# Kernel tuning notes

Hardware: AMD Instinct MI355X
Metric: run time of the kernel (lower is better)

The kernel has to match this reference:

```python
import jax, jax.numpy as jnp
import numpy as np

EMBED_DIM = 768
NUM_HEADS = 12
FF_DIM = 3072
HEAD_DIM = EMBED_DIM // NUM_HEADS
LN_EPS = 1e-5


def setup_inputs() -> dict:
    key = jax.random.key(0)
    ks = jax.random.split(key, 10)
    C, F = EMBED_DIM, FF_DIM
    s = lambda d: 1.0 / np.sqrt(d)
    return {
        "x": jax.random.normal(ks[0], (2, 2048, C), dtype=jnp.float32),
        "w_qkv": jax.random.normal(ks[1], (C, 3 * C), dtype=jnp.float32) * s(C),
        "w_out": jax.random.normal(ks[2], (C, C), dtype=jnp.float32) * s(C),
        "ln1_g": jnp.ones((C,), jnp.float32),
        "ln1_b": jnp.zeros((C,), jnp.float32),
        "ln2_g": jnp.ones((C,), jnp.float32),
        "ln2_b": jnp.zeros((C,), jnp.float32),
        "w1": jax.random.normal(ks[3], (C, F), dtype=jnp.float32) * s(C),
        "b1": jnp.zeros((F,), jnp.float32),
        "w2": jax.random.normal(ks[4], (F, C), dtype=jnp.float32) * s(F),
        "b2": jnp.zeros((C,), jnp.float32),
    }


def _layernorm(x, g, b):
    mu = jnp.mean(x, axis=-1, keepdims=True)
    var = jnp.var(x, axis=-1, keepdims=True)
    return (x - mu) * jax.lax.rsqrt(var + LN_EPS) * g + b


def _attention(x, w_qkv, w_out):
    B, T, C = x.shape
    qkv = x @ w_qkv                               # [B,T,3C]
    q, k, v = jnp.split(qkv, 3, axis=2)
    def heads(t):  # [B,T,C] -> [B,H,T,Dh]
        return t.reshape(B, T, NUM_HEADS, HEAD_DIM).transpose(0, 2, 1, 3)
    q, k, v = heads(q), heads(k), heads(v)
    att = jnp.einsum("bhqd,bhkd->bhqk", q, k) / np.sqrt(HEAD_DIM)
    mask = jnp.tril(jnp.ones((T, T), bool))
    att = jnp.where(mask, att, -jnp.inf)
    att = jax.nn.softmax(att, axis=-1)
    out = jnp.einsum("bhqk,bhkd->bhqd", att, v)   # [B,H,T,Dh]
    out = out.transpose(0, 2, 1, 3).reshape(B, T, C)
    return out @ w_out


def reference(x, w_qkv, w_out, ln1_g, ln1_b, ln2_g, ln2_b, w1, b1, w2, b2):
    x = x + _attention(_layernorm(x, ln1_g, ln1_b), w_qkv, w_out)
    h = _layernorm(x, ln2_g, ln2_b)
    h = jax.nn.gelu(h @ w1 + b1, approximate=False) @ w2 + b2
    return x + h
```

## Files before the change

kernel.cpp:

```cpp
#include <hip/hip_runtime.h>
#include <hip/hip_bf16.h>
#include <math.h>

typedef __attribute__((ext_vector_type(8))) short short8;
typedef __attribute__((ext_vector_type(4))) float f32x4;
typedef __attribute__((address_space(1))) const void CG;
typedef __attribute__((address_space(3))) void LS;

#define LOAD_LDS16(src, dst) __builtin_amdgcn_global_load_lds((CG*)(src), (LS*)(dst), 16, 0, 0)

__device__ __forceinline__ short f2bf(float f) {
  union { float f; unsigned u; } v; v.f = f;
  unsigned r = v.u + 0x7fffu + ((v.u >> 16) & 1u);
  return (short)(r >> 16);
}

__global__ __launch_bounds__(256) void transp_f32_bf16(const float* __restrict__ W,
                                                       short* __restrict__ Wt,
                                                       int K, int N) {
  __shared__ short t[32][33];
  int n0 = blockIdx.x << 5, k0 = blockIdx.y << 5;
  int tid = threadIdx.x;
#pragma unroll
  for (int p = 0; p < 4; ++p) {
    int e = tid + (p << 8);
    int r = e >> 5, c = e & 31;
    t[r][c] = f2bf(W[(size_t)(k0 + r) * N + n0 + c]);
  }
  __syncthreads();
#pragma unroll
  for (int p = 0; p < 4; ++p) {
    int e = tid + (p << 8);
    int r = e >> 5, c = e & 31;
    Wt[(size_t)(n0 + r) * K + k0 + c] = t[c][r];
  }
}

__global__ __launch_bounds__(256) void ln_kernel(const float* __restrict__ x,
                                                 const float* __restrict__ g,
                                                 const float* __restrict__ b,
                                                 short* __restrict__ out) {
  int row = blockIdx.x;
  const float* xr = x + (size_t)row * 768;
  int tid = threadIdx.x;
  float v0 = xr[tid], v1 = xr[tid + 256], v2 = xr[tid + 512];
  float s = v0 + v1 + v2;
  float ss = v0 * v0 + v1 * v1 + v2 * v2;
#pragma unroll
  for (int m = 1; m < 64; m <<= 1) { s += __shfl_xor(s, m); ss += __shfl_xor(ss, m); }
  __shared__ float red[8];
  int w = tid >> 6;
  if ((tid & 63) == 0) { red[w] = s; red[w + 4] = ss; }
  __syncthreads();
  s = red[0] + red[1] + red[2] + red[3];
  ss = red[4] + red[5] + red[6] + red[7];
  float mean = s * (1.0f / 768.0f);
  float var = ss * (1.0f / 768.0f) - mean * mean;
  float rs = rsqrtf(var + 1e-5f);
  short* outr = out + (size_t)row * 768;
  outr[tid]       = f2bf((v0 - mean) * rs * g[tid]       + b[tid]);
  outr[tid + 256] = f2bf((v1 - mean) * rs * g[tid + 256] + b[tid + 256]);
  outr[tid + 512] = f2bf((v2 - mean) * rs * g[tid + 512] + b[tid + 512]);
}

template <int EPI>
__global__ __launch_bounds__(256, 2) void gemm_bt(
    const short* __restrict__ A, const short* __restrict__ Bt,
    int M, int N, int K,
    short* __restrict__ outQ, short* __restrict__ outK, short* __restrict__ outVt,
    float* __restrict__ outF, short* __restrict__ outB,
    const float* __restrict__ bias, const float* __restrict__ resid) {
  __shared__ short lA[128 * 32];
  __shared__ short lB[128 * 32];
  int tid = threadIdx.x;
  int lane = tid & 63, w = tid >> 6;
  int li = lane & 15, g = lane >> 4;
  int bm = blockIdx.y << 7, bn = blockIdx.x << 7;
  int wrow = (w >> 1) << 6, wcol = (w & 1) << 6;

  const short* as[2];
  const short* bs[2];
#pragma unroll
  for (int p = 0; p < 2; ++p) {
    int v = tid + (p << 8);
    int row = v >> 2;
    int lc = (v & 3) ^ ((row ^ (row >> 2)) & 3);
    as[p] = A + (size_t)(bm + row) * K + lc * 8;
    bs[p] = Bt + (size_t)(bn + row) * K + lc * 8;
  }
  char* lAb = (char*)lA;
  char* lBb = (char*)lB;
  int sg = (g ^ ((li ^ (li >> 2)) & 3)) << 3;

  f32x4 zero = {0.f, 0.f, 0.f, 0.f};
  f32x4 acc[4][4];
#pragma unroll
  for (int i = 0; i < 4; ++i)
#pragma unroll
    for (int j = 0; j < 4; ++j) acc[i][j] = zero;

  for (int k0 = 0; k0 < K; k0 += 32) {
    __syncthreads();
#pragma unroll
    for (int p = 0; p < 2; ++p) {
      LOAD_LDS16(as[p] + k0, lAb + (p << 12) + (w << 10));
      LOAD_LDS16(bs[p] + k0, lBb + (p << 12) + (w << 10));
    }
    __syncthreads();
    short8 af[4], bf[4];
#pragma unroll
    for (int rt = 0; rt < 4; ++rt)
      af[rt] = *(const short8*)&lA[(wrow + rt * 16 + li) * 32 + sg];
#pragma unroll
    for (int ct = 0; ct < 4; ++ct)
      bf[ct] = *(const short8*)&lB[(wcol + ct * 16 + li) * 32 + sg];
#pragma unroll
    for (int rt = 0; rt < 4; ++rt)
#pragma unroll
      for (int ct = 0; ct < 4; ++ct)
        acc[rt][ct] = __builtin_amdgcn_mfma_f32_16x16x32_bf16(af[rt], bf[ct], acc[rt][ct], 0, 0, 0);
  }

#pragma unroll
  for (int rt = 0; rt < 4; ++rt) {
    int mbase = bm + wrow + rt * 16 + g * 4;
#pragma unroll
    for (int ct = 0; ct < 4; ++ct) {
      int n = bn + wcol + ct * 16 + li;
      f32x4 c = acc[rt][ct];
      if (EPI == 0) {
        if (n < 768) {
          int h = n >> 6, d = n & 63;
#pragma unroll
          for (int i = 0; i < 4; ++i) {
            int tok = mbase + i;
            int bb = tok >> 11, t = tok & 2047;
            outQ[((size_t)((bb * 12 + h) * 2048 + t) << 6) + d] = f2bf(c[i]);
          }
        } else if (n < 1536) {
          int nn = n - 768;
          int h = nn >> 6, d = nn & 63;
#pragma unroll
          for (int i = 0; i < 4; ++i) {
            int tok = mbase + i;
            int bb = tok >> 11, t = tok & 2047;
            outK[((size_t)((bb * 12 + h) * 2048 + t) << 6) + d] = f2bf(c[i]);
          }
        } else {
          int nn = n - 1536;
          int h = nn >> 6, d = nn & 63;
          int bb = mbase >> 11, t = mbase & 2047;
          ushort4 pk;
          pk.x = (unsigned short)f2bf(c[0]);
          pk.y = (unsigned short)f2bf(c[1]);
          pk.z = (unsigned short)f2bf(c[2]);
          pk.w = (unsigned short)f2bf(c[3]);
          *(ushort4*)((unsigned short*)outVt + (((size_t)((bb * 12 + h) * 64 + d)) << 11) + t) = pk;
        }
      } else if (EPI == 1) {
#pragma unroll
        for (int i = 0; i < 4; ++i) {
          int m = mbase + i;
          outF[(size_t)m * N + n] = c[i] + resid[(size_t)m * N + n];
        }
      } else if (EPI == 2) {
        float bv = bias[n];
#pragma unroll
        for (int i = 0; i < 4; ++i) {
          int m = mbase + i;
          float xx = c[i] + bv;
          float gel = 0.5f * xx * (1.0f + erff(xx * 0.70710678118654752f));
          outB[(size_t)m * N + n] = f2bf(gel);
        }
      } else {
        float bv = bias[n];
#pragma unroll
        for (int i = 0; i < 4; ++i) {
          int m = mbase + i;
          outF[(size_t)m * N + n] = c[i] + bv + resid[(size_t)m * N + n];
        }
      }
    }
  }
}

__global__ __launch_bounds__(256, 3) void attn_kernel(const short* __restrict__ Q,
                                                      const short* __restrict__ Kk,
                                                      const short* __restrict__ Vt,
                                                      short* __restrict__ O) {
  __shared__ short lK[2][64 * 64];
  __shared__ short lV[2][64 * 64];
  __shared__ short lP[4][32 * 64];
  int tid = threadIdx.x;
  int lane = tid & 63, w = tid >> 6;
  int li = lane & 15, g = lane >> 4;
  int bh = blockIdx.y;
  int qt = (int)gridDim.x - 1 - (int)blockIdx.x;
  int qbase = (qt << 7) + (w << 5);
  const short* Qb = Q + ((size_t)bh << 17);
  const short* Kb = Kk + ((size_t)bh << 17);
  const short* Vb = Vt + ((size_t)bh << 17);

  short8 qf[2][2];
#pragma unroll
  for (int rt = 0; rt < 2; ++rt)
#pragma unroll
    for (int kc = 0; kc < 2; ++kc)
      qf[rt][kc] = *(const short8*)&Qb[(size_t)(qbase + rt * 16 + li) * 64 + kc * 32 + g * 8];

  int r0 = tid >> 3, s0 = (tid & 7) ^ (r0 & 7);
  int r1 = r0 + 32,  s1 = (tid & 7) ^ (r1 & 7);
  const short* kS0 = Kb + r0 * 64 + s0 * 8;
  const short* kS1 = Kb + r1 * 64 + s1 * 8;
  const short* vS0 = Vb + (size_t)r0 * 2048 + s0 * 8;
  const short* vS1 = Vb + (size_t)r1 * 2048 + s1 * 8;

#define STAGE(buf, kt)                                                        \
  do {                                                                        \
    LOAD_LDS16(kS0 + (size_t)(kt) * 4096, (char*)lK[buf] + (w << 10));        \
    LOAD_LDS16(kS1 + (size_t)(kt) * 4096, (char*)lK[buf] + 4096 + (w << 10)); \
    LOAD_LDS16(vS0 + (size_t)(kt) * 64,   (char*)lV[buf] + (w << 10));        \
    LOAD_LDS16(vS1 + (size_t)(kt) * 64,   (char*)lV[buf] + 4096 + (w << 10)); \
  } while (0)

  const short8 kOnes = {0x3F80, 0x3F80, 0x3F80, 0x3F80, 0x3F80, 0x3F80, 0x3F80, 0x3F80};
  f32x4 zero = {0.f, 0.f, 0.f, 0.f};
  f32x4 o[2][4];
  f32x4 lrow[2];
  float mrow[2] = {-1e30f, -1e30f};
#pragma unroll
  for (int rt = 0; rt < 2; ++rt) {
    lrow[rt] = zero;
#pragma unroll
    for (int ct = 0; ct < 4; ++ct) o[rt][ct] = zero;
  }

  int diagKt = qbase >> 6;
  int nkt = (qt << 1) + 2;
  const float SCALE = 0.18033688011112042f;
  int sw = li & 7;

  STAGE(0, 0);

  for (int kt = 0; kt < nkt; ++kt) {
    int cur = kt & 1;
    __syncthreads();
    if (kt + 1 < nkt) STAGE(cur ^ 1, kt + 1);

    if (kt <= diagKt) {
      const short* Kc = lK[cur];
      const short* Vc = lV[cur];

      f32x4 s[2][4];
#pragma unroll
      for (int rt = 0; rt < 2; ++rt)
#pragma unroll
        for (int ct = 0; ct < 4; ++ct) s[rt][ct] = zero;
#pragma unroll
      for (int kc = 0; kc < 2; ++kc)
#pragma unroll
        for (int ct = 0; ct < 4; ++ct) {
          short8 kf = *(const short8*)&Kc[(ct * 16 + li) * 64 + ((((kc << 2) | g) ^ sw) << 3)];
#pragma unroll
          for (int rt = 0; rt < 2; ++rt)
            s[rt][ct] = __builtin_amdgcn_mfma_f32_16x16x32_bf16(qf[rt][kc], kf, s[rt][ct], 0, 0, 0);
        }

      if (kt == diagKt) {
        int kbase = kt << 6;
#pragma unroll
        for (int rt = 0; rt < 2; ++rt) {
          int qrow0 = qbase + rt * 16 + g * 4;
#pragma unroll
          for (int ct = 0; ct < 4; ++ct) {
            int kcol = kbase + ct * 16 + li;
#pragma unroll
            for (int i = 0; i < 4; ++i)
              if (kcol > qrow0 + i) s[rt][ct][i] = -1e30f;
          }
        }
      }

      unsigned short* Pw = (unsigned short*)lP[w];
#pragma unroll
      for (int rt = 0; rt < 2; ++rt) {
        float tm = s[rt][0][0];
#pragma unroll
        for (int ct = 0; ct < 4; ++ct)
#pragma unroll
          for (int i = 0; i < 4; ++i) tm = fmaxf(tm, s[rt][ct][i]);
#pragma unroll
        for (int m2 = 1; m2 < 64; m2 <<= 1) tm = fmaxf(tm, __shfl_xor(tm, m2));
        if (tm > mrow[rt] + 8.0f) {
          float corr = exp2f((mrow[rt] - tm) * SCALE);
          mrow[rt] = tm;
#pragma unroll
          for (int i = 0; i < 4; ++i) lrow[rt][i] *= corr;
#pragma unroll
          for (int ct = 0; ct < 4; ++ct)
#pragma unroll
            for (int i = 0; i < 4; ++i) o[rt][ct][i] *= corr;
        }
#pragma unroll
        for (int ct = 0; ct < 4; ++ct)
#pragma unroll
          for (int i = 0; i < 4; ++i) {
            float p = exp2f((s[rt][ct][i] - mrow[rt]) * SCALE);
            int row = rt * 16 + (g << 2) + i;
            int col = (ct << 4) + li;
            int ch = (col >> 3) ^ (row & 7);
            Pw[(row << 6) + (ch << 3) + (col & 7)] = (unsigned short)f2bf(p);
          }
      }

      f32x4 psum[2];
      psum[0] = zero; psum[1] = zero;
#pragma unroll
      for (int kc = 0; kc < 2; ++kc) {
        short8 vf[4];
#pragma unroll
        for (int ct = 0; ct < 4; ++ct)
          vf[ct] = *(const short8*)&Vc[(ct * 16 + li) * 64 + ((((kc << 2) | g) ^ sw) << 3)];
#pragma unroll
        for (int rt = 0; rt < 2; ++rt) {
          short8 pf = *(const short8*)&lP[w][(rt * 16 + li) * 64 + ((((kc << 2) | g) ^ sw) << 3)];
#pragma unroll
          for (int ct = 0; ct < 4; ++ct)
            o[rt][ct] = __builtin_amdgcn_mfma_f32_16x16x32_bf16(pf, vf[ct], o[rt][ct], 0, 0, 0);
          psum[rt] = __builtin_amdgcn_mfma_f32_16x16x32_bf16(pf, kOnes, psum[rt], 0, 0, 0);
        }
      }
#pragma unroll
      for (int rt = 0; rt < 2; ++rt)
#pragma unroll
        for (int i = 0; i < 4; ++i) lrow[rt][i] += psum[rt][i];
    }
  }
#undef STAGE

  int b = bh / 12, h = bh % 12;
#pragma unroll
  for (int rt = 0; rt < 2; ++rt)
#pragma unroll
    for (int i = 0; i < 4; ++i) {
      float inv = 1.0f / lrow[rt][i];
      int t = qbase + rt * 16 + g * 4 + i;
      size_t base = ((size_t)(b * 2048 + t)) * 768 + h * 64;
#pragma unroll
      for (int ct = 0; ct < 4; ++ct)
        O[base + ct * 16 + li] = f2bf(o[rt][ct][i] * inv);
    }
}

extern "C" void kernel_launch(void* const* d_in, const int* in_sizes, int n_in,
                              void* d_out, int out_size, void* d_ws, size_t ws_size,
                              hipStream_t stream) {
  const float* x     = (const float*)d_in[0];
  const float* w_qkv = (const float*)d_in[1];
  const float* w_out = (const float*)d_in[2];
  const float* ln1g  = (const float*)d_in[3];
  const float* ln1b  = (const float*)d_in[4];
  const float* ln2g  = (const float*)d_in[5];
  const float* ln2b  = (const float*)d_in[6];
  const float* w1    = (const float*)d_in[7];
  const float* b1    = (const float*)d_in[8];
  const float* w2    = (const float*)d_in[9];
  const float* b2    = (const float*)d_in[10];
  float* out = (float*)d_out;
  char* ws = (char*)d_ws;

  short* wqkvT = (short*)(ws + 0);
  short* woutT = (short*)(ws + 3538944);
  short* w1T   = (short*)(ws + 4718592);
  short* w2T   = (short*)(ws + 9437184);
  short* qb    = (short*)(ws + 14155776);
  short* kb    = (short*)(ws + 20447232);
  short* vtb   = (short*)(ws + 26738688);
  short* attnb = (short*)(ws + 33030144);
  short* ab    = qb;
  short* xnb   = (short*)(ws + 39321600);
  float* x2b   = (float*)(ws + 45613056);

  transp_f32_bf16<<<dim3(72, 24), 256, 0, stream>>>(w_qkv, wqkvT, 768, 2304);
  transp_f32_bf16<<<dim3(24, 24), 256, 0, stream>>>(w_out, woutT, 768, 768);
  transp_f32_bf16<<<dim3(96, 24), 256, 0, stream>>>(w1, w1T, 768, 3072);
  transp_f32_bf16<<<dim3(24, 96), 256, 0, stream>>>(w2, w2T, 3072, 768);

  ln_kernel<<<dim3(4096), 256, 0, stream>>>(x, ln1g, ln1b, xnb);

  gemm_bt<0><<<dim3(18, 32), 256, 0, stream>>>(xnb, wqkvT, 4096, 2304, 768,
                                               qb, kb, vtb, nullptr, nullptr, nullptr, nullptr);

  attn_kernel<<<dim3(16, 24), 256, 0, stream>>>(qb, kb, vtb, attnb);

  gemm_bt<1><<<dim3(6, 32), 256, 0, stream>>>(attnb, woutT, 4096, 768, 768,
                                              nullptr, nullptr, nullptr, x2b, nullptr, nullptr, x);

  ln_kernel<<<dim3(4096), 256, 0, stream>>>(x2b, ln2g, ln2b, xnb);

  gemm_bt<2><<<dim3(24, 32), 256, 0, stream>>>(xnb, w1T, 4096, 3072, 768,
                                               nullptr, nullptr, nullptr, nullptr, ab, b1, nullptr);

  gemm_bt<3><<<dim3(6, 32), 256, 0, stream>>>(ab, w2T, 4096, 768, 3072,
                                              nullptr, nullptr, nullptr, out, nullptr, b2, x2b);
}
```

Measured before the change: 271.7 us.

## Split attention KV across waves, split-K the FF2 GEMM, fuse weight transposes

The attention kernel now gives each block 32 query rows and splits the causal key range across its four waves. Each wave reads K and V straight from global memory instead of staging them in LDS, and the partial softmax states are merged through shared memory. The grid grows to 64x24 blocks to raise parallelism and balance causal work. The final FF2 GEMM is split over K into two halves that accumulate into the output with atomicAdd after a memset, and the four weight-transpose launches become one kernel. The trade-offs are more global-memory and L2 traffic for K and V, atomic contention, an extra memset, and non-deterministic float summation order.

```diff
diff --git a/kernel.cpp b/kernel.cpp
--- a/kernel.cpp
+++ b/kernel.cpp
@@ -15,11 +15,22 @@
   return (short)(r >> 16);
 }
 
-__global__ __launch_bounds__(256) void transp_f32_bf16(const float* __restrict__ W,
-                                                       short* __restrict__ Wt,
-                                                       int K, int N) {
+__global__ __launch_bounds__(256) void transp_all(const float* __restrict__ w_qkv,
+                                                  const float* __restrict__ w_out,
+                                                  const float* __restrict__ w1,
+                                                  const float* __restrict__ w2,
+                                                  short* __restrict__ wqkvT,
+                                                  short* __restrict__ woutT,
+                                                  short* __restrict__ w1T,
+                                                  short* __restrict__ w2T) {
   __shared__ short t[32][33];
-  int n0 = blockIdx.x << 5, k0 = blockIdx.y << 5;
+  int bid = blockIdx.x;
+  const float* W; short* Wt; int K, N, nx, id;
+  if (bid < 1728)      { W = w_qkv; Wt = wqkvT; K = 768;  N = 2304; nx = 72; id = bid; }
+  else if (bid < 2304) { W = w_out; Wt = woutT; K = 768;  N = 768;  nx = 24; id = bid - 1728; }
+  else if (bid < 4608) { W = w1;    Wt = w1T;   K = 768;  N = 3072; nx = 96; id = bid - 2304; }
+  else                 { W = w2;    Wt = w2T;   K = 3072; N = 768;  nx = 24; id = bid - 4608; }
+  int n0 = (id % nx) << 5, k0 = (id / nx) << 5;
   int tid = threadIdx.x;
 #pragma unroll
   for (int p = 0; p < 4; ++p) {
@@ -77,6 +88,8 @@
   int li = lane & 15, g = lane >> 4;
   int bm = blockIdx.y << 7, bn = blockIdx.x << 7;
   int wrow = (w >> 1) << 6, wcol = (w & 1) << 6;
+  size_t lda = (EPI == 4) ? 3072 : (size_t)K;
+  int koff = (EPI == 4) ? (int)blockIdx.z * 1536 : 0;
 
   const short* as[2];
   const short* bs[2];
@@ -85,8 +98,8 @@
     int v = tid + (p << 8);
     int row = v >> 2;
     int lc = (v & 3) ^ ((row ^ (row >> 2)) & 3);
-    as[p] = A + (size_t)(bm + row) * K + lc * 8;
-    bs[p] = Bt + (size_t)(bn + row) * K + lc * 8;
+    as[p] = A + (size_t)(bm + row) * lda + koff + lc * 8;
+    bs[p] = Bt + (size_t)(bn + row) * lda + koff + lc * 8;
   }
   char* lAb = (char*)lA;
   char* lBb = (char*)lB;
@@ -172,12 +185,21 @@
           float gel = 0.5f * xx * (1.0f + erff(xx * 0.70710678118654752f));
           outB[(size_t)m * N + n] = f2bf(gel);
         }
-      } else {
+      } else if (EPI == 3) {
         float bv = bias[n];
 #pragma unroll
         for (int i = 0; i < 4; ++i) {
           int m = mbase + i;
           outF[(size_t)m * N + n] = c[i] + bv + resid[(size_t)m * N + n];
+        }
+      } else {
+        bool last = (blockIdx.z == 1);
+        float bv = last ? bias[n] : 0.f;
+#pragma unroll
+        for (int i = 0; i < 4; ++i) {
+          int m = mbase + i;
+          float add = c[i] + bv + (last ? resid[(size_t)m * N + n] : 0.f);
+          atomicAdd(&outF[(size_t)m * N + n], add);
         }
       }
     }
@@ -188,15 +210,16 @@
                                                       const short* __restrict__ Kk,
                                                       const short* __restrict__ Vt,
                                                       short* __restrict__ O) {
-  __shared__ short lK[2][64 * 64];
-  __shared__ short lV[2][64 * 64];
   __shared__ short lP[4][32 * 64];
+  __shared__ float cO[2][32][68];
+  __shared__ float cL[2][32];
+  __shared__ float cM[2][2];
   int tid = threadIdx.x;
   int lane = tid & 63, w = tid >> 6;
   int li = lane & 15, g = lane >> 4;
   int bh = blockIdx.y;
-  int qt = (int)gridDim.x - 1 - (int)blockIdx.x;
-  int qbase = (qt << 7) + (w << 5);
+  int qi = 63 - (int)blockIdx.x;
+  int qbase = qi << 5;
   const short* Qb = Q + ((size_t)bh << 17);
   const short* Kb = Kk + ((size_t)bh << 17);
   const short* Vb = Vt + ((size_t)bh << 17);
@@ -207,21 +230,6 @@
 #pragma unroll
     for (int kc = 0; kc < 2; ++kc)
       qf[rt][kc] = *(const short8*)&Qb[(size_t)(qbase + rt * 16 + li) * 64 + kc * 32 + g * 8];
-
-  int r0 = tid >> 3, s0 = (tid & 7) ^ (r0 & 7);
-  int r1 = r0 + 32,  s1 = (tid & 7) ^ (r1 & 7);
-  const short* kS0 = Kb + r0 * 64 + s0 * 8;
-  const short* kS1 = Kb + r1 * 64 + s1 * 8;
-  const short* vS0 = Vb + (size_t)r0 * 2048 + s0 * 8;
-  const short* vS1 = Vb + (size_t)r1 * 2048 + s1 * 8;
-
-#define STAGE(buf, kt)                                                        \
-  do {                                                                        \
-    LOAD_LDS16(kS0 + (size_t)(kt) * 4096, (char*)lK[buf] + (w << 10));        \
-    LOAD_LDS16(kS1 + (size_t)(kt) * 4096, (char*)lK[buf] + 4096 + (w << 10)); \
-    LOAD_LDS16(vS0 + (size_t)(kt) * 64,   (char*)lV[buf] + (w << 10));        \
-    LOAD_LDS16(vS1 + (size_t)(kt) * 64,   (char*)lV[buf] + 4096 + (w << 10)); \
-  } while (0)
 
   const short8 kOnes = {0x3F80, 0x3F80, 0x3F80, 0x3F80, 0x3F80, 0x3F80, 0x3F80, 0x3F80};
   f32x4 zero = {0.f, 0.f, 0.f, 0.f};
@@ -235,121 +243,172 @@
     for (int ct = 0; ct < 4; ++ct) o[rt][ct] = zero;
   }
 
-  int diagKt = qbase >> 6;
-  int nkt = (qt << 1) + 2;
+  int nkt = (qi >> 1) + 1;
+  int cs = (nkt + 3) >> 2;
+  int kbeg = w * cs;
+  int kend = kbeg + cs; if (kend > nkt) kend = nkt;
   const float SCALE = 0.18033688011112042f;
   int sw = li & 7;
-
-  STAGE(0, 0);
-
-  for (int kt = 0; kt < nkt; ++kt) {
-    int cur = kt & 1;
-    __syncthreads();
-    if (kt + 1 < nkt) STAGE(cur ^ 1, kt + 1);
-
-    if (kt <= diagKt) {
-      const short* Kc = lK[cur];
-      const short* Vc = lV[cur];
-
-      f32x4 s[2][4];
-#pragma unroll
-      for (int rt = 0; rt < 2; ++rt)
-#pragma unroll
-        for (int ct = 0; ct < 4; ++ct) s[rt][ct] = zero;
-#pragma unroll
-      for (int kc = 0; kc < 2; ++kc)
+  unsigned short* Pw = (unsigned short*)lP[w];
+
+  for (int kt = kbeg; kt < kend; ++kt) {
+    f32x4 s[2][4];
+#pragma unroll
+    for (int rt = 0; rt < 2; ++rt)
+#pragma unroll
+      for (int ct = 0; ct < 4; ++ct) s[rt][ct] = zero;
+#pragma unroll
+    for (int kc = 0; kc < 2; ++kc)
+#pragma unroll
+      for (int ct = 0; ct < 4; ++ct) {
+        short8 kf = *(const short8*)&Kb[(size_t)(kt * 64 + ct * 16 + li) * 64 + kc * 32 + g * 8];
+#pragma unroll
+        for (int rt = 0; rt < 2; ++rt)
+          s[rt][ct] = __builtin_amdgcn_mfma_f32_16x16x32_bf16(qf[rt][kc], kf, s[rt][ct], 0, 0, 0);
+      }
+
+    if (kt == nkt - 1) {
+      int kb0 = kt << 6;
+#pragma unroll
+      for (int rt = 0; rt < 2; ++rt) {
+        int qrow0 = qbase + rt * 16 + g * 4;
 #pragma unroll
         for (int ct = 0; ct < 4; ++ct) {
-          short8 kf = *(const short8*)&Kc[(ct * 16 + li) * 64 + ((((kc << 2) | g) ^ sw) << 3)];
-#pragma unroll
-          for (int rt = 0; rt < 2; ++rt)
-            s[rt][ct] = __builtin_amdgcn_mfma_f32_16x16x32_bf16(qf[rt][kc], kf, s[rt][ct], 0, 0, 0);
-        }
-
-      if (kt == diagKt) {
-        int kbase = kt << 6;
-#pragma unroll
-        for (int rt = 0; rt < 2; ++rt) {
-          int qrow0 = qbase + rt * 16 + g * 4;
-#pragma unroll
-          for (int ct = 0; ct < 4; ++ct) {
-            int kcol = kbase + ct * 16 + li;
-#pragma unroll
-            for (int i = 0; i < 4; ++i)
-              if (kcol > qrow0 + i) s[rt][ct][i] = -1e30f;
-          }
-        }
-      }
-
-      unsigned short* Pw = (unsigned short*)lP[w];
+          int kcol = kb0 + ct * 16 + li;
+#pragma unroll
+          for (int i = 0; i < 4; ++i)
+            if (kcol > qrow0 + i) s[rt][ct][i] = -1e30f;
+        }
+      }
+    }
+
+#pragma unroll
+    for (int rt = 0; rt < 2; ++rt) {
+      float tm = s[rt][0][0];
+#pragma unroll
+      for (int ct = 0; ct < 4; ++ct)
+#pragma unroll
+        for (int i = 0; i < 4; ++i) tm = fmaxf(tm, s[rt][ct][i]);
+#pragma unroll
+      for (int m2 = 1; m2 < 64; m2 <<= 1) tm = fmaxf(tm, __shfl_xor(tm, m2));
+      if (tm > mrow[rt] + 8.0f) {
+        float corr = exp2f((mrow[rt] - tm) * SCALE);
+        mrow[rt] = tm;
+#pragma unroll
+        for (int i = 0; i < 4; ++i) lrow[rt][i] *= corr;
+#pragma unroll
+        for (int ct = 0; ct < 4; ++ct)
+#pragma unroll
+          for (int i = 0; i < 4; ++i) o[rt][ct][i] *= corr;
+      }
+#pragma unroll
+      for (int ct = 0; ct < 4; ++ct)
+#pragma unroll
+        for (int i = 0; i < 4; ++i) {
+          float p = exp2f((s[rt][ct][i] - mrow[rt]) * SCALE);
+          int row = rt * 16 + (g << 2) + i;
+          int col = (ct << 4) + li;
+          int ch = (col >> 3) ^ (row & 7);
+          Pw[(row << 6) + (ch << 3) + (col & 7)] = (unsigned short)f2bf(p);
+        }
+    }
+
+    f32x4 psum[2];
+    psum[0] = zero; psum[1] = zero;
+#pragma unroll
+    for (int kc = 0; kc < 2; ++kc) {
+      short8 vf[4];
+#pragma unroll
+      for (int ct = 0; ct < 4; ++ct)
+        vf[ct] = *(const short8*)&Vb[(size_t)(ct * 16 + li) * 2048 + kt * 64 + kc * 32 + g * 8];
 #pragma unroll
       for (int rt = 0; rt < 2; ++rt) {
-        float tm = s[rt][0][0];
+        short8 pf = *(const short8*)&lP[w][(rt * 16 + li) * 64 + ((((kc << 2) | g) ^ sw) << 3)];
 #pragma unroll
         for (int ct = 0; ct < 4; ++ct)
-#pragma unroll
-          for (int i = 0; i < 4; ++i) tm = fmaxf(tm, s[rt][ct][i]);
-#pragma unroll
-        for (int m2 = 1; m2 < 64; m2 <<= 1) tm = fmaxf(tm, __shfl_xor(tm, m2));
-        if (tm > mrow[rt] + 8.0f) {
-          float corr = exp2f((mrow[rt] - tm) * SCALE);
-          mrow[rt] = tm;
-#pragma unroll
-          for (int i = 0; i < 4; ++i) lrow[rt][i] *= corr;
-#pragma unroll
-          for (int ct = 0; ct < 4; ++ct)
-#pragma unroll
-            for (int i = 0; i < 4; ++i) o[rt][ct][i] *= corr;
-        }
+          o[rt][ct] = __builtin_amdgcn_mfma_f32_16x16x32_bf16(pf, vf[ct], o[rt][ct], 0, 0, 0);
+        psum[rt] = __builtin_amdgcn_mfma_f32_16x16x32_bf16(pf, kOnes, psum[rt], 0, 0, 0);
+      }
+    }
+#pragma unroll
+    for (int rt = 0; rt < 2; ++rt)
+#pragma unroll
+      for (int i = 0; i < 4; ++i) lrow[rt][i] += psum[rt][i];
+  }
+
+  __syncthreads();
+  if (w >= 2) {
+    int slot = w - 2;
+#pragma unroll
+    for (int rt = 0; rt < 2; ++rt) {
+      if (lane == 0) cM[slot][rt] = mrow[rt];
+#pragma unroll
+      for (int i = 0; i < 4; ++i) {
+        int row = rt * 16 + (g << 2) + i;
+        if (li == 0) cL[slot][row] = lrow[rt][i];
+#pragma unroll
+        for (int ct = 0; ct < 4; ++ct) cO[slot][row][ct * 16 + li] = o[rt][ct][i];
+      }
+    }
+  }
+  __syncthreads();
+  if (w < 2) {
+    int slot = w;
+#pragma unroll
+    for (int rt = 0; rt < 2; ++rt) {
+      float ms = cM[slot][rt];
+      float m2 = fmaxf(mrow[rt], ms);
+      float fu = exp2f((mrow[rt] - m2) * SCALE);
+      float fs = exp2f((ms - m2) * SCALE);
+      mrow[rt] = m2;
+#pragma unroll
+      for (int i = 0; i < 4; ++i) {
+        int row = rt * 16 + (g << 2) + i;
+        lrow[rt][i] = lrow[rt][i] * fu + cL[slot][row] * fs;
 #pragma unroll
         for (int ct = 0; ct < 4; ++ct)
-#pragma unroll
-          for (int i = 0; i < 4; ++i) {
-            float p = exp2f((s[rt][ct][i] - mrow[rt]) * SCALE);
-            int row = rt * 16 + (g << 2) + i;
-            int col = (ct << 4) + li;
-            int ch = (col >> 3) ^ (row & 7);
-            Pw[(row << 6) + (ch << 3) + (col & 7)] = (unsigned short)f2bf(p);
-          }
-      }
-
-      f32x4 psum[2];
-      psum[0] = zero; psum[1] = zero;
-#pragma unroll
-      for (int kc = 0; kc < 2; ++kc) {
-        short8 vf[4];
-#pragma unroll
-        for (int ct = 0; ct < 4; ++ct)
-          vf[ct] = *(const short8*)&Vc[(ct * 16 + li) * 64 + ((((kc << 2) | g) ^ sw) << 3)];
-#pragma unroll
-        for (int rt = 0; rt < 2; ++rt) {
-          short8 pf = *(const short8*)&lP[w][(rt * 16 + li) * 64 + ((((kc << 2) | g) ^ sw) << 3)];
-#pragma unroll
-          for (int ct = 0; ct < 4; ++ct)
-            o[rt][ct] = __builtin_amdgcn_mfma_f32_16x16x32_bf16(pf, vf[ct], o[rt][ct], 0, 0, 0);
-          psum[rt] = __builtin_amdgcn_mfma_f32_16x16x32_bf16(pf, kOnes, psum[rt], 0, 0, 0);
-        }
-      }
-#pragma unroll
-      for (int rt = 0; rt < 2; ++rt)
-#pragma unroll
-        for (int i = 0; i < 4; ++i) lrow[rt][i] += psum[rt][i];
-    }
-  }
-#undef STAGE
-
-  int b = bh / 12, h = bh % 12;
-#pragma unroll
-  for (int rt = 0; rt < 2; ++rt)
-#pragma unroll
-    for (int i = 0; i < 4; ++i) {
-      float inv = 1.0f / lrow[rt][i];
-      int t = qbase + rt * 16 + g * 4 + i;
-      size_t base = ((size_t)(b * 2048 + t)) * 768 + h * 64;
-#pragma unroll
-      for (int ct = 0; ct < 4; ++ct)
-        O[base + ct * 16 + li] = f2bf(o[rt][ct][i] * inv);
-    }
+          o[rt][ct][i] = o[rt][ct][i] * fu + cO[slot][row][ct * 16 + li] * fs;
+      }
+    }
+  }
+  __syncthreads();
+  if (w == 1) {
+#pragma unroll
+    for (int rt = 0; rt < 2; ++rt) {
+      if (lane == 0) cM[0][rt] = mrow[rt];
+#pragma unroll
+      for (int i = 0; i < 4; ++i) {
+        int row = rt * 16 + (g << 2) + i;
+        if (li == 0) cL[0][row] = lrow[rt][i];
+#pragma unroll
+        for (int ct = 0; ct < 4; ++ct) cO[0][row][ct * 16 + li] = o[rt][ct][i];
+      }
+    }
+  }
+  __syncthreads();
+  if (w == 0) {
+    int b = bh / 12, h = bh % 12;
+#pragma unroll
+    for (int rt = 0; rt < 2; ++rt) {
+      float ms = cM[0][rt];
+      float m2 = fmaxf(mrow[rt], ms);
+      float fu = exp2f((mrow[rt] - m2) * SCALE);
+      float fs = exp2f((ms - m2) * SCALE);
+#pragma unroll
+      for (int i = 0; i < 4; ++i) {
+        int row = rt * 16 + (g << 2) + i;
+        float l2 = lrow[rt][i] * fu + cL[0][row] * fs;
+        float inv = 1.0f / l2;
+        int t = qbase + row;
+        size_t base = ((size_t)(b * 2048 + t)) * 768 + h * 64;
+#pragma unroll
+        for (int ct = 0; ct < 4; ++ct) {
+          float ov = o[rt][ct][i] * fu + cO[0][row][ct * 16 + li] * fs;
+          O[base + ct * 16 + li] = f2bf(ov * inv);
+        }
+      }
+    }
+  }
 }
 
 extern "C" void kernel_launch(void* const* d_in, const int* in_sizes, int n_in,
@@ -381,17 +440,14 @@
   short* xnb   = (short*)(ws + 39321600);
   float* x2b   = (float*)(ws + 45613056);
 
-  transp_f32_bf16<<<dim3(72, 24), 256, 0, stream>>>(w_qkv, wqkvT, 768, 2304);
-  transp_f32_bf16<<<dim3(24, 24), 256, 0, stream>>>(w_out, woutT, 768, 768);
-  transp_f32_bf16<<<dim3(96, 24), 256, 0, stream>>>(w1, w1T, 768, 3072);
-  transp_f32_bf16<<<dim3(24, 96), 256, 0, stream>>>(w2, w2T, 3072, 768);
+  transp_all<<<dim3(6912), 256, 0, stream>>>(w_qkv, w_out, w1, w2, wqkvT, woutT, w1T, w2T);
 
   ln_kernel<<<dim3(4096), 256, 0, stream>>>(x, ln1g, ln1b, xnb);
 
   gemm_bt<0><<<dim3(18, 32), 256, 0, stream>>>(xnb, wqkvT, 4096, 2304, 768,
                                                qb, kb, vtb, nullptr, nullptr, nullptr, nullptr);
 
-  attn_kernel<<<dim3(16, 24), 256, 0, stream>>>(qb, kb, vtb, attnb);
+  attn_kernel<<<dim3(64, 24), 256, 0, stream>>>(qb, kb, vtb, attnb);
 
   gemm_bt<1><<<dim3(6, 32), 256, 0, stream>>>(attnb, woutT, 4096, 768, 768,
                                               nullptr, nullptr, nullptr, x2b, nullptr, nullptr, x);
@@ -401,6 +457,7 @@
   gemm_bt<2><<<dim3(24, 32), 256, 0, stream>>>(xnb, w1T, 4096, 3072, 768,
                                                nullptr, nullptr, nullptr, nullptr, ab, b1, nullptr);
 
-  gemm_bt<3><<<dim3(6, 32), 256, 0, stream>>>(ab, w2T, 4096, 768, 3072,
-                                              nullptr, nullptr, nullptr, out, nullptr, b2, x2b);
-}
+  hipMemsetAsync(out, 0, (size_t)4096 * 768 * 4, stream);
+  gemm_bt<4><<<dim3(6, 32, 2), 256, 0, stream>>>(ab, w2T, 4096, 768, 1536,
+                                                 nullptr, nullptr, nullptr, out, nullptr, b2, x2b);
+}
```

Result: slower. 278.4 us (+2.5%).

## Split attention KV range across blocks, split-K final GEMM, merge transpose launches

Applied to the files above, without the earlier changes.

Attention now runs as 40 chunk-blocks per head. Longer causal query tiles have their KV range split into up to four chunks, and each chunk writes bf16 partial outputs plus per-row max and sum. A new combine kernel rescales and merges these partials. The FF2 GEMM is split into two K halves that accumulate into a zeroed output with atomics, and the four weight-transpose launches become one. The aim is to fill the 256 CUs better on small grids, at the cost of extra partial-output traffic, bf16 rounding of partials, a memset, and atomic adds.

```diff
diff --git a/kernel.cpp b/kernel.cpp
--- a/kernel.cpp
+++ b/kernel.cpp
@@ -15,11 +15,22 @@
   return (short)(r >> 16);
 }
 
-__global__ __launch_bounds__(256) void transp_f32_bf16(const float* __restrict__ W,
-                                                       short* __restrict__ Wt,
-                                                       int K, int N) {
+__global__ __launch_bounds__(256) void transp_all(const float* __restrict__ w_qkv,
+                                                  const float* __restrict__ w_out,
+                                                  const float* __restrict__ w1,
+                                                  const float* __restrict__ w2,
+                                                  short* __restrict__ wqkvT,
+                                                  short* __restrict__ woutT,
+                                                  short* __restrict__ w1T,
+                                                  short* __restrict__ w2T) {
   __shared__ short t[32][33];
-  int n0 = blockIdx.x << 5, k0 = blockIdx.y << 5;
+  int bid = blockIdx.x;
+  const float* W; short* Wt; int K, N, nx, id;
+  if (bid < 1728)      { W = w_qkv; Wt = wqkvT; K = 768;  N = 2304; nx = 72; id = bid; }
+  else if (bid < 2304) { W = w_out; Wt = woutT; K = 768;  N = 768;  nx = 24; id = bid - 1728; }
+  else if (bid < 4608) { W = w1;    Wt = w1T;   K = 768;  N = 3072; nx = 96; id = bid - 2304; }
+  else                 { W = w2;    Wt = w2T;   K = 3072; N = 768;  nx = 24; id = bid - 4608; }
+  int n0 = (id % nx) << 5, k0 = (id / nx) << 5;
   int tid = threadIdx.x;
 #pragma unroll
   for (int p = 0; p < 4; ++p) {
@@ -77,6 +88,8 @@
   int li = lane & 15, g = lane >> 4;
   int bm = blockIdx.y << 7, bn = blockIdx.x << 7;
   int wrow = (w >> 1) << 6, wcol = (w & 1) << 6;
+  size_t lda = (EPI == 4) ? 3072 : (size_t)K;
+  int koff = (EPI == 4) ? (int)blockIdx.z * 1536 : 0;
 
   const short* as[2];
   const short* bs[2];
@@ -85,8 +98,8 @@
     int v = tid + (p << 8);
     int row = v >> 2;
     int lc = (v & 3) ^ ((row ^ (row >> 2)) & 3);
-    as[p] = A + (size_t)(bm + row) * K + lc * 8;
-    bs[p] = Bt + (size_t)(bn + row) * K + lc * 8;
+    as[p] = A + (size_t)(bm + row) * lda + koff + lc * 8;
+    bs[p] = Bt + (size_t)(bn + row) * lda + koff + lc * 8;
   }
   char* lAb = (char*)lA;
   char* lBb = (char*)lB;
@@ -172,13 +185,22 @@
           float gel = 0.5f * xx * (1.0f + erff(xx * 0.70710678118654752f));
           outB[(size_t)m * N + n] = f2bf(gel);
         }
-      } else {
+      } else if (EPI == 3) {
         float bv = bias[n];
 #pragma unroll
         for (int i = 0; i < 4; ++i) {
           int m = mbase + i;
           outF[(size_t)m * N + n] = c[i] + bv + resid[(size_t)m * N + n];
         }
+      } else {
+        bool last = (blockIdx.z == 1);
+        float bv = last ? bias[n] : 0.f;
+#pragma unroll
+        for (int i = 0; i < 4; ++i) {
+          int m = mbase + i;
+          float add = c[i] + bv + (last ? resid[(size_t)m * N + n] : 0.f);
+          atomicAdd(&outF[(size_t)m * N + n], add);
+        }
       }
     }
   }
@@ -187,7 +209,8 @@
 __global__ __launch_bounds__(256, 3) void attn_kernel(const short* __restrict__ Q,
                                                       const short* __restrict__ Kk,
                                                       const short* __restrict__ Vt,
-                                                      short* __restrict__ O) {
+                                                      unsigned short* __restrict__ o_part,
+                                                      float* __restrict__ ml_part) {
   __shared__ short lK[2][64 * 64];
   __shared__ short lV[2][64 * 64];
   __shared__ short lP[4][32 * 64];
@@ -195,7 +218,16 @@
   int lane = tid & 63, w = tid >> 6;
   int li = lane & 15, g = lane >> 4;
   int bh = blockIdx.y;
-  int qt = (int)gridDim.x - 1 - (int)blockIdx.x;
+  int cid = 39 - (int)blockIdx.x;
+  int qt = 0, cum = 0;
+  while (true) { int n = (qt >> 2) + 1; if (cid < cum + n) break; cum += n; ++qt; }
+  int c = cid - cum;
+  int nch = (qt >> 2) + 1;
+  int nt = (qt + 1) << 1;
+  int bq = nt / nch, rem = nt % nch;
+  int t0 = c * bq + (c < rem ? c : rem);
+  int t1 = t0 + bq + (c < rem ? 1 : 0);
+
   int qbase = (qt << 7) + (w << 5);
   const short* Qb = Q + ((size_t)bh << 17);
   const short* Kb = Kk + ((size_t)bh << 17);
@@ -236,16 +268,16 @@
   }
 
   int diagKt = qbase >> 6;
-  int nkt = (qt << 1) + 2;
   const float SCALE = 0.18033688011112042f;
   int sw = li & 7;
-
-  STAGE(0, 0);
-
-  for (int kt = 0; kt < nkt; ++kt) {
-    int cur = kt & 1;
+  unsigned short* Pw = (unsigned short*)lP[w];
+
+  STAGE(0, t0);
+
+  for (int kt = t0; kt < t1; ++kt) {
+    int cur = (kt - t0) & 1;
     __syncthreads();
-    if (kt + 1 < nkt) STAGE(cur ^ 1, kt + 1);
+    if (kt + 1 < t1) STAGE(cur ^ 1, kt + 1);
 
     if (kt <= diagKt) {
       const short* Kc = lK[cur];
@@ -267,13 +299,13 @@
         }
 
       if (kt == diagKt) {
-        int kbase = kt << 6;
+        int kb0 = kt << 6;
 #pragma unroll
         for (int rt = 0; rt < 2; ++rt) {
           int qrow0 = qbase + rt * 16 + g * 4;
 #pragma unroll
           for (int ct = 0; ct < 4; ++ct) {
-            int kcol = kbase + ct * 16 + li;
+            int kcol = kb0 + ct * 16 + li;
 #pragma unroll
             for (int i = 0; i < 4; ++i)
               if (kcol > qrow0 + i) s[rt][ct][i] = -1e30f;
@@ -281,7 +313,6 @@
         }
       }
 
-      unsigned short* Pw = (unsigned short*)lP[w];
 #pragma unroll
       for (int rt = 0; rt < 2; ++rt) {
         float tm = s[rt][0][0];
@@ -338,18 +369,87 @@
   }
 #undef STAGE
 
+  int pid = bh * 40 + cid;
+#pragma unroll
+  for (int rt = 0; rt < 2; ++rt)
+#pragma unroll
+    for (int ct = 0; ct < 4; ++ct) {
+      int col = (ct << 4) + li;
+      int row0 = (w << 5) + (rt << 4) + (g << 2);
+      ushort4 pk;
+      pk.x = (unsigned short)f2bf(o[rt][ct][0]);
+      pk.y = (unsigned short)f2bf(o[rt][ct][1]);
+      pk.z = (unsigned short)f2bf(o[rt][ct][2]);
+      pk.w = (unsigned short)f2bf(o[rt][ct][3]);
+      *(ushort4*)&o_part[((size_t)pid * 64 + col) * 128 + row0] = pk;
+    }
+  if (li == 0) {
+    float2* mlp = (float2*)ml_part;
+#pragma unroll
+    for (int rt = 0; rt < 2; ++rt)
+#pragma unroll
+      for (int i = 0; i < 4; ++i) {
+        int row = (w << 5) + (rt << 4) + (g << 2) + i;
+        mlp[(size_t)pid * 128 + row] = make_float2(mrow[rt], lrow[rt][i]);
+      }
+  }
+}
+
+__global__ __launch_bounds__(256) void attn_combine(const unsigned short* __restrict__ o_part,
+                                                    const float* __restrict__ ml_part,
+                                                    short* __restrict__ O) {
+  __shared__ float wgt[4][128];
+  int qt = blockIdx.x, bh = blockIdx.y;
+  int a = qt >> 2, bb = qt & 3;
+  int c0 = 2 * a * (a - 1) + a * bb + qt;
+  int nch = a + 1;
+  int pid0 = bh * 40 + c0;
+  int tid = threadIdx.x;
+  const float SCALE = 0.18033688011112042f;
+  const float2* mlp = (const float2*)ml_part;
+
+  if (tid < 128) {
+    int row = tid;
+    float mv[4] = {-1e30f, -1e30f, -1e30f, -1e30f};
+    float lv[4] = {0.f, 0.f, 0.f, 0.f};
+#pragma unroll
+    for (int c = 0; c < 4; ++c)
+      if (c < nch) {
+        float2 ml = mlp[(size_t)(pid0 + c) * 128 + row];
+        mv[c] = ml.x; lv[c] = ml.y;
+      }
+    float M = fmaxf(fmaxf(mv[0], mv[1]), fmaxf(mv[2], mv[3]));
+    float u[4];
+    float L = 0.f;
+#pragma unroll
+    for (int c = 0; c < 4; ++c) {
+      u[c] = (c < nch) ? exp2f((mv[c] - M) * SCALE) : 0.f;
+      L += lv[c] * u[c];
+    }
+    float inv = 1.0f / L;
+#pragma unroll
+    for (int c = 0; c < 4; ++c) wgt[c][row] = u[c] * inv;
+  }
+  __syncthreads();
+
+  int col = tid & 63, rg = tid >> 6;
   int b = bh / 12, h = bh % 12;
-#pragma unroll
-  for (int rt = 0; rt < 2; ++rt)
-#pragma unroll
-    for (int i = 0; i < 4; ++i) {
-      float inv = 1.0f / lrow[rt][i];
-      int t = qbase + rt * 16 + g * 4 + i;
-      size_t base = ((size_t)(b * 2048 + t)) * 768 + h * 64;
-#pragma unroll
-      for (int ct = 0; ct < 4; ++ct)
-        O[base + ct * 16 + li] = f2bf(o[rt][ct][i] * inv);
-    }
+  size_t obase[4];
+#pragma unroll
+  for (int c = 0; c < 4; ++c) obase[c] = ((size_t)(pid0 + c) * 64 + col) * 128;
+  for (int r = 0; r < 32; ++r) {
+    int row = (rg << 5) + r;
+    float acc = 0.f;
+#pragma unroll
+    for (int c = 0; c < 4; ++c)
+      if (c < nch) {
+        union { unsigned u; float f; } cv;
+        cv.u = ((unsigned)o_part[obase[c] + row]) << 16;
+        acc += cv.f * wgt[c][row];
+      }
+    int t = (qt << 7) + row;
+    O[((size_t)(b * 2048 + t)) * 768 + h * 64 + col] = f2bf(acc);
+  }
 }
 
 extern "C" void kernel_launch(void* const* d_in, const int* in_sizes, int n_in,
@@ -380,18 +480,18 @@
   short* ab    = qb;
   short* xnb   = (short*)(ws + 39321600);
   float* x2b   = (float*)(ws + 45613056);
-
-  transp_f32_bf16<<<dim3(72, 24), 256, 0, stream>>>(w_qkv, wqkvT, 768, 2304);
-  transp_f32_bf16<<<dim3(24, 24), 256, 0, stream>>>(w_out, woutT, 768, 768);
-  transp_f32_bf16<<<dim3(96, 24), 256, 0, stream>>>(w1, w1T, 768, 3072);
-  transp_f32_bf16<<<dim3(24, 96), 256, 0, stream>>>(w2, w2T, 3072, 768);
+  unsigned short* o_part = (unsigned short*)(ws + 39321600);
+  float* ml_part = (float*)(ws + 55050240);
+
+  transp_all<<<dim3(6912), 256, 0, stream>>>(w_qkv, w_out, w1, w2, wqkvT, woutT, w1T, w2T);
 
   ln_kernel<<<dim3(4096), 256, 0, stream>>>(x, ln1g, ln1b, xnb);
 
   gemm_bt<0><<<dim3(18, 32), 256, 0, stream>>>(xnb, wqkvT, 4096, 2304, 768,
                                                qb, kb, vtb, nullptr, nullptr, nullptr, nullptr);
 
-  attn_kernel<<<dim3(16, 24), 256, 0, stream>>>(qb, kb, vtb, attnb);
+  attn_kernel<<<dim3(40, 24), 256, 0, stream>>>(qb, kb, vtb, o_part, ml_part);
+  attn_combine<<<dim3(16, 24), 256, 0, stream>>>(o_part, ml_part, attnb);
 
   gemm_bt<1><<<dim3(6, 32), 256, 0, stream>>>(attnb, woutT, 4096, 768, 768,
                                               nullptr, nullptr, nullptr, x2b, nullptr, nullptr, x);
@@ -401,6 +501,7 @@
   gemm_bt<2><<<dim3(24, 32), 256, 0, stream>>>(xnb, w1T, 4096, 3072, 768,
                                                nullptr, nullptr, nullptr, nullptr, ab, b1, nullptr);
 
-  gemm_bt<3><<<dim3(6, 32), 256, 0, stream>>>(ab, w2T, 4096, 768, 3072,
-                                              nullptr, nullptr, nullptr, out, nullptr, b2, x2b);
-}
+  hipMemsetAsync(out, 0, (size_t)4096 * 768 * 4, stream);
+  gemm_bt<4><<<dim3(6, 32, 2), 256, 0, stream>>>(ab, w2T, 4096, 768, 1536,
+                                                 nullptr, nullptr, nullptr, out, nullptr, b2, x2b);
+}
```

Measured after the change: 255.9 us. -5.8%, faster.
